# Kernel optimization log

Hardware: AMD Instinct MI355X
Metric: run time of the kernel (lower is better)

## Reference

```python
import jax, jax.numpy as jnp
import numpy as np


def setup_inputs() -> dict:
    key = jax.random.key(0)
    B, D, C, H = 4096, 64, 128, 512
    ks = jax.random.split(key, 6)
    return {
        "q_z_x_params": jax.random.normal(ks[0], (B, C), jnp.float32),
        "eps": jax.random.normal(ks[1], (B, D), jnp.float32),
        "W1": jax.random.normal(ks[2], (D + C, H), jnp.float32) / np.sqrt(D + C).astype(np.float32),
        "b1": jnp.zeros((H,), jnp.float32),
        "W2": jax.random.normal(ks[3], (H, H), jnp.float32) / np.sqrt(H).astype(np.float32),
        "b2": jnp.zeros((H,), jnp.float32),
        "W3": jax.random.normal(ks[4], (H, 2 * D), jnp.float32) / np.sqrt(H).astype(np.float32),
        "b3": jnp.zeros((2 * D,), jnp.float32),
    }


def _made_masks(D, C, H):
    # Standard MADE degrees, natural ordering; context columns fully connected.
    m_in = np.arange(1, D + 1)                      # input degrees 1..D
    m_h = (np.arange(H) % (D - 1)) + 1              # hidden degrees 1..D-1
    M1 = np.concatenate([m_h[None, :] >= m_in[:, None],
                         np.ones((C, H), bool)], axis=0)   # (D+C, H)
    M2 = m_h[None, :] >= m_h[:, None]               # (H, H)
    m_out = np.tile(np.arange(1, D + 1), 2)         # (2D,) mean||prescale
    M3 = m_out[None, :] > m_h[:, None]              # (H, 2D)
    f32 = jnp.float32
    return jnp.asarray(M1, f32), jnp.asarray(M2, f32), jnp.asarray(M3, f32)


def reference(q_z_x_params, eps, W1, b1, W2, b2, W3, b3):
    B, D = eps.shape
    C = q_z_x_params.shape[1]
    H = W2.shape[0]
    M1, M2, M3 = _made_masks(D, C, H)
    mW1, mW2, mW3 = W1 * M1, W2 * M2, W3 * M3

    def made(z):
        x = jnp.concatenate([z, q_z_x_params], axis=1)   # (B, D+C)
        h1 = jax.nn.relu(x @ mW1 + b1)
        h2 = jax.nn.relu(h1 @ mW2 + b2)
        out = h2 @ mW3 + b3                              # (B, 2D)
        return out[:, :D], out[:, D:]

    def step(z, i):
        mean, prescale = made(z)
        mu_i = jnp.take(mean, i, axis=1)                 # (B,)
        scale_i = jax.nn.softplus(jnp.take(prescale, i, axis=1))
        z_i = mu_i + scale_i * jnp.take(eps, i, axis=1)  # reparameterized Normal sample
        z = z.at[:, i].set(z_i)
        return z, None

    z0 = jnp.zeros((B, D), eps.dtype)
    z_sample, _ = jax.lax.scan(step, z0, jnp.arange(D))
    return z_sample
```

## Files before the change

kernel.cpp:

```cpp
#include <hip/hip_runtime.h>
#include <math.h>

#define DD 64
#define CC 128
#define HH 512
#define BATCH 4096

typedef __attribute__((ext_vector_type(2))) float f32x2;

__device__ __forceinline__ f32x2 splat2(float x) { f32x2 v; v[0] = x; v[1] = x; return v; }

__device__ __forceinline__ float fast_softplus(float x) {
    float t = exp2f(-fabsf(x) * 1.44269504f);
    return fmaxf(x, 0.f) + 0.69314718f * log2f(1.f + t);
}

__device__ __forceinline__ float bcast(float x, int l) {
    return __int_as_float(__builtin_amdgcn_readlane(__float_as_int(x), l));
}

typedef const __attribute__((address_space(1))) void* as1_cptr;
typedef __attribute__((address_space(3))) void* as3_ptr;
__device__ __forceinline__ void glds16(const float* g, float* l) {
    __builtin_amdgcn_global_load_lds((as1_cptr)g, (as3_ptr)l, 16, 0, 0);
}

__global__ __launch_bounds__(256, 2) void made_sample(
    const float* __restrict__ ctx,
    const float* __restrict__ eps,
    const float* __restrict__ W1,
    const float* __restrict__ b1,
    const float* __restrict__ W2,
    const float* __restrict__ b2,
    const float* __restrict__ W3,
    const float* __restrict__ b3,
    float* __restrict__ out)
{
    const int lane  = threadIdx.x & 63;
    const int w     = threadIdx.x >> 6;
    const int rbase = blockIdx.x * 8 + w * 2;
    const int jbase = 8 * lane;

    __shared__ float sbuf[2][10 * HH];

    int deg[8];
    #pragma unroll
    for (int u = 0; u < 8; ++u) deg[u] = (jbase + u) % 63 + 1;

    auto load8v = [&](const float* base_, f32x2* r_) {
        float4 a = *(const float4*)(base_ + lane * 4);
        float4 b = *(const float4*)(base_ + 256 + lane * 4);
        r_[0][0] = a.x; r_[0][1] = a.y; r_[1][0] = a.z; r_[1][1] = a.w;
        r_[2][0] = b.x; r_[2][1] = b.y; r_[3][0] = b.z; r_[3][1] = b.w;
    };
    auto stage_row = [&](const float* src, float* dst) {
        glds16(src + lane * 8,     dst);
        glds16(src + lane * 8 + 4, dst + 256);
    };

    f32x2 p1[2][4], p2[2][4], acc[2];
    #pragma unroll
    for (int j = 0; j < 4; ++j) {
        f32x2 t1, t2;
        t1[0] = b1[jbase + 2 * j]; t1[1] = b1[jbase + 2 * j + 1];
        t2[0] = b2[jbase + 2 * j]; t2[1] = b2[jbase + 2 * j + 1];
        p1[0][j] = t1; p1[1][j] = t1;
        p2[0][j] = t2; p2[1][j] = t2;
    }
    acc[0] = splat2(0.f);
    acc[1] = splat2(0.f);

    float ca[2], cb[2], ep[2];
    #pragma unroll
    for (int r = 0; r < 2; ++r) {
        ca[r] = ctx[(rbase + r) * CC + lane];
        cb[r] = ctx[(rbase + r) * CC + 64 + lane];
        ep[r] = eps[(rbase + r) * DD + lane];
    }
    const float b3m = b3[lane];
    const float b3p = b3[64 + lane];

    auto stage_ctx = [&](int ch, float* buf) {
        #pragma unroll
        for (int q2 = 0; q2 < 2; ++q2) {
            const int q = 2 * w + q2;
            stage_row(W1 + (DD + 8 * ch + q) * HH, buf + q * HH);
        }
    };
    auto stage_step = [&](int in, float* buf) {
        const int basen = (in == 0) ? 0 : (in - 1);
        #pragma unroll
        for (int rr = 0; rr < 3; ++rr) {
            const int r = w + 4 * rr;
            if (r <= 9) {
                const float* src;
                if (r < 9) {
                    int k = basen + 63 * r;
                    if (k >= HH) k = HH - 8;
                    src = W2 + k * HH;
                } else {
                    src = W1 + in * HH;
                }
                stage_row(src, buf + r * HH);
            }
        }
    };

    stage_ctx(0, sbuf[0]);
    __syncthreads();
    #pragma unroll 1
    for (int ch = 0; ch < 16; ++ch) {
        float* cur = sbuf[ch & 1];
        float* nxt = sbuf[(ch + 1) & 1];
        if (ch < 15) stage_ctx(ch + 1, nxt);
        else         stage_step(0, sbuf[0]);
        #pragma unroll
        for (int q = 0; q < 8; ++q) {
            f32x2 wv[4];
            load8v(cur + q * HH, wv);
            const int c = 8 * ch + q;
            #pragma unroll
            for (int r = 0; r < 2; ++r) {
                const float cv = bcast((ch < 8) ? ca[r] : cb[r], c & 63);
                const f32x2 cv2 = splat2(cv);
                #pragma unroll
                for (int j = 0; j < 4; ++j) p1[r][j] += cv2 * wv[j];
            }
        }
        __syncthreads();
    }

    float z[2] = {0.f, 0.f};

    #pragma unroll 1
    for (int i = 0; i < DD; ++i) {
        float* cur = sbuf[i & 1];
        float* nxt = sbuf[(i + 1) & 1];
        if (i < 63) stage_step(i + 1, nxt);

        const int base = (i == 0) ? 0 : (i - 1);

        f32x2 w3v[9];
        #pragma unroll
        for (int t = 0; t < 9; ++t) {
            const int k  = base + 63 * t;
            const int ks = (k < HH) ? k : (HH - 1);
            w3v[t][0] = W3[ks * (2 * DD) + lane];
            w3v[t][1] = W3[ks * (2 * DD) + 64 + lane];
        }

        float m[2];
        #pragma unroll
        for (int r = 0; r < 2; ++r) {
            float mv = 0.f;
            #pragma unroll
            for (int u = 0; u < 8; ++u)
                mv = (deg[u] == i) ? p1[r][u >> 1][u & 1] : mv;
            m[r] = fmaxf(mv, 0.f);
        }

        #pragma unroll
        for (int t = 0; t < 9; ++t) {
            const int k = base + 63 * t;
            f32x2 wv[4];
            load8v(cur + t * HH, wv);
            float h0, h1v;
            if (t == 8) {
                const float vm = (k < HH) ? 1.f : 0.f;
                h0  = vm * bcast(m[0], 63);
                h1v = vm * bcast(m[1], 63);
            } else {
                h0  = bcast(m[0], k >> 3);
                h1v = bcast(m[1], k >> 3);
            }
            const f32x2 h0v = splat2(h0), h1vv = splat2(h1v);
            #pragma unroll
            for (int j = 0; j < 4; ++j) {
                p2[0][j] += h0v  * wv[j];
                p2[1][j] += h1vv * wv[j];
            }
        }

        float hn[2];
        #pragma unroll
        for (int r = 0; r < 2; ++r) {
            float hv = 0.f;
            #pragma unroll
            for (int u = 0; u < 8; ++u)
                hv = (deg[u] == i) ? p2[r][u >> 1][u & 1] : hv;
            hn[r] = fmaxf(hv, 0.f);
        }

        #pragma unroll
        for (int t = 0; t < 9; ++t) {
            const int k = base + 63 * t;
            float h0, h1v;
            if (t == 8) {
                const float vm = (k < HH) ? 1.f : 0.f;
                h0  = vm * bcast(hn[0], 63);
                h1v = vm * bcast(hn[1], 63);
            } else {
                h0  = bcast(hn[0], k >> 3);
                h1v = bcast(hn[1], k >> 3);
            }
            acc[0] += splat2(h0)  * w3v[t];
            acc[1] += splat2(h1v) * w3v[t];
        }

        f32x2 w1v[4];
        load8v(cur + 9 * HH, w1v);
        #pragma unroll
        for (int r = 0; r < 2; ++r) {
            const float am = acc[r][0] + b3m;
            const float ap = acc[r][1] + b3p;
            const float sp = fast_softplus(ap);
            const float zc = fmaf(sp, ep[r], am);
            const float zi = bcast(zc, i);
            if (lane == i) z[r] = zi;
            const f32x2 zi2 = splat2(zi);
            #pragma unroll
            for (int j = 0; j < 4; ++j) p1[r][j] += zi2 * w1v[j];
        }

        __syncthreads();
    }

    #pragma unroll
    for (int r = 0; r < 2; ++r) out[(rbase + r) * DD + lane] = z[r];
}

extern "C" void kernel_launch(void* const* d_in, const int* in_sizes, int n_in,
                              void* d_out, int out_size, void* d_ws, size_t ws_size,
                              hipStream_t stream) {
    const float* ctx = (const float*)d_in[0];
    const float* eps = (const float*)d_in[1];
    const float* W1  = (const float*)d_in[2];
    const float* b1  = (const float*)d_in[3];
    const float* W2  = (const float*)d_in[4];
    const float* b2  = (const float*)d_in[5];
    const float* W3  = (const float*)d_in[6];
    const float* b3  = (const float*)d_in[7];
    (void)d_ws; (void)ws_size; (void)in_sizes; (void)n_in; (void)out_size;

    made_sample<<<BATCH / 8, 256, 0, stream>>>(ctx, eps, W1, b1, W2, b2, W3, b3,
                                               (float*)d_out);
}
```

Measured before the change: 184.7 us.

## Triple-buffer W2 staging two steps ahead and register-prefetch W3/W1 rows

Moves the per-step W2 staging to a three-slot LDS ring filled two steps ahead. W3 and W1 rows now go straight into double-buffered registers one step ahead instead of through LDS. The end-of-step __syncthreads is replaced by a raw waitcnt plus s_barrier, which lets outstanding global loads stay in flight across the barrier. This targets load latency exposed on the serial 64-step critical path, at the cost of more registers and LDS (3x9 rows), which may lower occupancy under the launch bound of 2.

```diff
diff --git a/kernel.cpp b/kernel.cpp
--- a/kernel.cpp
+++ b/kernel.cpp
@@ -24,6 +24,9 @@
 __device__ __forceinline__ void glds16(const float* g, float* l) {
     __builtin_amdgcn_global_load_lds((as1_cptr)g, (as3_ptr)l, 16, 0, 0);
 }
+
+#define ROWF 512
+#define BUF_F (9 * ROWF)
 
 __global__ __launch_bounds__(256, 2) void made_sample(
     const float* __restrict__ ctx,
@@ -41,21 +44,17 @@
     const int rbase = blockIdx.x * 8 + w * 2;
     const int jbase = 8 * lane;
 
-    __shared__ float sbuf[2][10 * HH];
+    __shared__ float sbuf[3][BUF_F];
 
     int deg[8];
     #pragma unroll
     for (int u = 0; u < 8; ++u) deg[u] = (jbase + u) % 63 + 1;
 
-    auto load8v = [&](const float* base_, f32x2* r_) {
+    auto ldrow = [&](const float* base_, f32x2* r_) {
         float4 a = *(const float4*)(base_ + lane * 4);
         float4 b = *(const float4*)(base_ + 256 + lane * 4);
         r_[0][0] = a.x; r_[0][1] = a.y; r_[1][0] = a.z; r_[1][1] = a.w;
         r_[2][0] = b.x; r_[2][1] = b.y; r_[3][0] = b.z; r_[3][1] = b.w;
-    };
-    auto stage_row = [&](const float* src, float* dst) {
-        glds16(src + lane * 8,     dst);
-        glds16(src + lane * 8 + 4, dst + 256);
     };
 
     f32x2 p1[2][4], p2[2][4], acc[2];
@@ -82,133 +81,122 @@
 
     auto stage_ctx = [&](int ch, float* buf) {
         #pragma unroll
-        for (int q2 = 0; q2 < 2; ++q2) {
-            const int q = 2 * w + q2;
-            stage_row(W1 + (DD + 8 * ch + q) * HH, buf + q * HH);
+        for (int q4 = 0; q4 < 4; ++q4) {
+            const int o = 4 * q4 + w;
+            const int q = o >> 1, hf = o & 1;
+            glds16(W1 + (DD + 8 * ch + q) * HH + lane * 8 + hf * 4,
+                   buf + q * ROWF + hf * 256);
         }
     };
     auto stage_step = [&](int in, float* buf) {
         const int basen = (in == 0) ? 0 : (in - 1);
         #pragma unroll
-        for (int rr = 0; rr < 3; ++rr) {
-            const int r = w + 4 * rr;
-            if (r <= 9) {
-                const float* src;
-                if (r < 9) {
-                    int k = basen + 63 * r;
-                    if (k >= HH) k = HH - 8;
-                    src = W2 + k * HH;
-                } else {
-                    src = W1 + in * HH;
-                }
-                stage_row(src, buf + r * HH);
-            }
-        }
-    };
-
-    stage_ctx(0, sbuf[0]);
+        for (int q5 = 0; q5 < 5; ++q5) {
+            const int o = 4 * q5 + w;
+            const int oc = (o < 18) ? o : (o - 2);
+            const int t = oc >> 1, hf = oc & 1;
+            int k = basen + 63 * t;
+            if (k >= HH) k = HH - 1;
+            glds16(W2 + k * HH + lane * 8 + hf * 4, buf + t * ROWF + hf * 256);
+        }
+    };
+    auto loadW3W1 = [&](int in, f32x2* w3v, f32x2* w1v) {
+        const int basen = (in == 0) ? 0 : (in - 1);
+        #pragma unroll
+        for (int t = 0; t < 9; ++t) {
+            int k = basen + 63 * t;
+            if (k >= HH) k = HH - 1;
+            w3v[t][0] = W3[k * (2 * DD) + lane];
+            w3v[t][1] = W3[k * (2 * DD) + 64 + lane];
+        }
+        float4 a = *(const float4*)(W1 + in * HH + lane * 8);
+        float4 b = *(const float4*)(W1 + in * HH + lane * 8 + 4);
+        w1v[0][0] = a.x; w1v[0][1] = a.y; w1v[1][0] = a.z; w1v[1][1] = a.w;
+        w1v[2][0] = b.x; w1v[2][1] = b.y; w1v[3][0] = b.z; w1v[3][1] = b.w;
+    };
+
+    stage_ctx(0, &sbuf[0][0]);
     __syncthreads();
     #pragma unroll 1
     for (int ch = 0; ch < 16; ++ch) {
-        float* cur = sbuf[ch & 1];
-        float* nxt = sbuf[(ch + 1) & 1];
-        if (ch < 15) stage_ctx(ch + 1, nxt);
-        else         stage_step(0, sbuf[0]);
+        float* cur = &sbuf[ch % 3][0];
+        if (ch < 15)  stage_ctx(ch + 1, &sbuf[(ch + 1) % 3][0]);
+        if (ch == 14) stage_step(0, &sbuf[1][0]);
+        if (ch == 15) stage_step(1, &sbuf[2][0]);
         #pragma unroll
         for (int q = 0; q < 8; ++q) {
             f32x2 wv[4];
-            load8v(cur + q * HH, wv);
+            ldrow(cur + q * ROWF, wv);
             const int c = 8 * ch + q;
             #pragma unroll
             for (int r = 0; r < 2; ++r) {
-                const float cv = bcast((ch < 8) ? ca[r] : cb[r], c & 63);
-                const f32x2 cv2 = splat2(cv);
+                const f32x2 cv = splat2(bcast((ch < 8) ? ca[r] : cb[r], c & 63));
                 #pragma unroll
-                for (int j = 0; j < 4; ++j) p1[r][j] += cv2 * wv[j];
+                for (int j = 0; j < 4; ++j) p1[r][j] += cv * wv[j];
             }
         }
         __syncthreads();
     }
 
+    f32x2 w3s[2][9], w1s[2][4];
+    loadW3W1(0, w3s[0], w1s[0]);
     float z[2] = {0.f, 0.f};
 
-    #pragma unroll 1
+    #pragma unroll 2
     for (int i = 0; i < DD; ++i) {
-        float* cur = sbuf[i & 1];
-        float* nxt = sbuf[(i + 1) & 1];
-        if (i < 63) stage_step(i + 1, nxt);
-
+        const int cs = i & 1;
+        float* cur = &sbuf[(i + 1) % 3][0];
+        if (i < 63) {
+            loadW3W1(i + 1, w3s[cs ^ 1], w1s[cs ^ 1]);
+            stage_step(i + 2, &sbuf[(i + 3) % 3][0]);
+        }
         const int base = (i == 0) ? 0 : (i - 1);
-
-        f32x2 w3v[9];
+        const float vm8 = (base + 504 < HH) ? 1.f : 0.f;
+
+        float m0 = 0.f, m1 = 0.f;
+        #pragma unroll
+        for (int u = 0; u < 8; ++u) {
+            const bool hit = (deg[u] == i);
+            m0 = hit ? p1[0][u >> 1][u & 1] : m0;
+            m1 = hit ? p1[1][u >> 1][u & 1] : m1;
+        }
+        m0 = fmaxf(m0, 0.f);
+        m1 = fmaxf(m1, 0.f);
+
         #pragma unroll
         for (int t = 0; t < 9; ++t) {
-            const int k  = base + 63 * t;
-            const int ks = (k < HH) ? k : (HH - 1);
-            w3v[t][0] = W3[ks * (2 * DD) + lane];
-            w3v[t][1] = W3[ks * (2 * DD) + 64 + lane];
-        }
-
-        float m[2];
-        #pragma unroll
-        for (int r = 0; r < 2; ++r) {
-            float mv = 0.f;
-            #pragma unroll
-            for (int u = 0; u < 8; ++u)
-                mv = (deg[u] == i) ? p1[r][u >> 1][u & 1] : mv;
-            m[r] = fmaxf(mv, 0.f);
-        }
-
-        #pragma unroll
-        for (int t = 0; t < 9; ++t) {
-            const int k = base + 63 * t;
             f32x2 wv[4];
-            load8v(cur + t * HH, wv);
-            float h0, h1v;
-            if (t == 8) {
-                const float vm = (k < HH) ? 1.f : 0.f;
-                h0  = vm * bcast(m[0], 63);
-                h1v = vm * bcast(m[1], 63);
-            } else {
-                h0  = bcast(m[0], k >> 3);
-                h1v = bcast(m[1], k >> 3);
-            }
-            const f32x2 h0v = splat2(h0), h1vv = splat2(h1v);
+            ldrow(cur + t * ROWF, wv);
+            const int ln = (t == 8) ? 63 : ((base + 63 * t) >> 3);
+            float h0 = bcast(m0, ln), h1 = bcast(m1, ln);
+            if (t == 8) { h0 *= vm8; h1 *= vm8; }
+            const f32x2 h0v = splat2(h0), h1v = splat2(h1);
             #pragma unroll
             for (int j = 0; j < 4; ++j) {
-                p2[0][j] += h0v  * wv[j];
-                p2[1][j] += h1vv * wv[j];
+                p2[0][j] += h0v * wv[j];
+                p2[1][j] += h1v * wv[j];
             }
         }
 
-        float hn[2];
-        #pragma unroll
-        for (int r = 0; r < 2; ++r) {
-            float hv = 0.f;
-            #pragma unroll
-            for (int u = 0; u < 8; ++u)
-                hv = (deg[u] == i) ? p2[r][u >> 1][u & 1] : hv;
-            hn[r] = fmaxf(hv, 0.f);
-        }
+        float hn0 = 0.f, hn1 = 0.f;
+        #pragma unroll
+        for (int u = 0; u < 8; ++u) {
+            const bool hit = (deg[u] == i);
+            hn0 = hit ? p2[0][u >> 1][u & 1] : hn0;
+            hn1 = hit ? p2[1][u >> 1][u & 1] : hn1;
+        }
+        hn0 = fmaxf(hn0, 0.f);
+        hn1 = fmaxf(hn1, 0.f);
 
         #pragma unroll
         for (int t = 0; t < 9; ++t) {
-            const int k = base + 63 * t;
-            float h0, h1v;
-            if (t == 8) {
-                const float vm = (k < HH) ? 1.f : 0.f;
-                h0  = vm * bcast(hn[0], 63);
-                h1v = vm * bcast(hn[1], 63);
-            } else {
-                h0  = bcast(hn[0], k >> 3);
-                h1v = bcast(hn[1], k >> 3);
-            }
-            acc[0] += splat2(h0)  * w3v[t];
-            acc[1] += splat2(h1v) * w3v[t];
-        }
-
-        f32x2 w1v[4];
-        load8v(cur + 9 * HH, w1v);
+            const int ln = (t == 8) ? 63 : ((base + 63 * t) >> 3);
+            float h0 = bcast(hn0, ln), h1 = bcast(hn1, ln);
+            if (t == 8) { h0 *= vm8; h1 *= vm8; }
+            acc[0] += splat2(h0) * w3s[cs][t];
+            acc[1] += splat2(h1) * w3s[cs][t];
+        }
+
         #pragma unroll
         for (int r = 0; r < 2; ++r) {
             const float am = acc[r][0] + b3m;
@@ -219,10 +207,13 @@
             if (lane == i) z[r] = zi;
             const f32x2 zi2 = splat2(zi);
             #pragma unroll
-            for (int j = 0; j < 4; ++j) p1[r][j] += zi2 * w1v[j];
-        }
-
-        __syncthreads();
+            for (int j = 0; j < 4; ++j) p1[r][j] += zi2 * w1s[cs][j];
+        }
+
+        if (i < 63) {
+            __builtin_amdgcn_s_waitcnt(0x0075);
+            __builtin_amdgcn_s_barrier();
+        }
     }
 
     #pragma unroll
```

Result: slower. 191.4 us (+3.7%).
